# Kernel tuning notes

Hardware: AMD Instinct MI355X
Metric: run time of the kernel (lower is better)

Reference implementation:

```python
import math
import jax, jax.numpy as jnp
import numpy as np

N_NODES = 50000
N_EDGES = 800000
F_IN = 512
HID = 64
N_CLS = 64
NITER = 10


def setup_inputs() -> dict:
    key = jax.random.key(0)
    k = jax.random.split(key, 6)
    x = jax.random.normal(k[0], (N_NODES, F_IN), jnp.float32)
    edge_index = jax.random.randint(k[1], (2, N_EDGES), 0, N_NODES, jnp.int64)
    W1 = jax.random.normal(k[2], (F_IN, HID), jnp.float32) / np.sqrt(F_IN)
    b1 = jnp.zeros((HID,), jnp.float32)
    W2 = jax.random.normal(k[3], (HID, N_CLS), jnp.float32) / np.sqrt(HID)
    b2 = jnp.zeros((N_CLS,), jnp.float32)
    halt_w = jax.random.normal(k[4], (N_CLS,), jnp.float32) / np.sqrt(N_CLS)
    # reset_parameters: bias = log((1/(niter+1)) / (1 - 1/(niter+1)))
    b = math.log((1.0 / (NITER + 1)) / (1.0 - 1.0 / (NITER + 1)))
    halt_b = jnp.full((1,), b, jnp.float32)
    return {"x": x, "edge_index": edge_index, "W1": W1, "b1": b1,
            "W2": W2, "b2": b2, "halt_w": halt_w, "halt_b": halt_b}


def reference(x, edge_index, W1, b1, W2, b2, halt_w, halt_b):
    N = x.shape[0]
    # MLP (eval mode: dropout is identity)
    h = jnp.maximum(x @ W1 + b1, 0.0)
    local = h @ W2 + b2                      # [N, C] local predictions
    # GCN normalization with self-loops (eval: no edge dropout)
    loops = jnp.arange(N, dtype=edge_index.dtype)
    row = jnp.concatenate([edge_index[0], loops])
    col = jnp.concatenate([edge_index[1], loops])
    deg = jnp.zeros((N,), x.dtype).at[row].add(1.0)
    dis = jnp.where(deg > 0, jax.lax.rsqrt(jnp.maximum(deg, 1.0)), 0.0)
    norm = dis[row] * dis[col]               # [E+N]

    def step(carry, _):
        prop, steps, sum_h, cont, xacc = carry
        old = prop
        msg = norm[:, None] * prop[row]                       # gather + scale
        prop = jax.ops.segment_sum(msg, col, num_segments=N)  # scatter-add
        hh = jax.nn.sigmoid(prop @ halt_w + halt_b[0])        # [N]
        prob = (sum_h + hh < 0.99) & cont
        pf = prob.astype(x.dtype)
        steps = steps + pf
        sum_h = sum_h + pf * hh
        cond = prob & (steps < NITER)
        p = jnp.where(cond, sum_h, 1.0 - sum_h)
        xacc = xacc + (prop * p[:, None] + old * (1.0 - p)[:, None]) * cont.astype(x.dtype)[:, None]
        cont = cont & prob
        return (prop, steps, sum_h, cont, xacc), None

    init = (local, jnp.ones((N,), x.dtype), jnp.zeros((N,), x.dtype),
            jnp.ones((N,), bool), jnp.zeros_like(local))
    (prop, steps, sum_h, cont, xacc), _ = jax.lax.scan(step, init, None, length=NITER)
    out = xacc / steps[:, None]
    return jax.nn.log_softmax(out, axis=1), steps, 1.0 - sum_h
```

## Files before the change

kernel.cpp:

```cpp
#include <hip/hip_runtime.h>
#include <hip/hip_bf16.h>

#define F_IN 512
#define NC 64
#define NITER 10

__global__ __launch_bounds__(256) void init_state_kernel(
    float* __restrict__ steps, float* __restrict__ sumh, int* __restrict__ cont,
    int* __restrict__ rowptr, int N, int E) {
  int i = blockIdx.x * blockDim.x + threadIdx.x;
  if (i < N) { steps[i] = 1.0f; sumh[i] = 0.0f; cont[i] = 1; }
  if (i == 0) rowptr[N] = E;
}

__global__ __launch_bounds__(256) void mlp_kernel(
    const float* __restrict__ x, const float* __restrict__ W1,
    const float* __restrict__ b1, const float* __restrict__ W2,
    const float* __restrict__ b2, float* __restrict__ out, int N) {
  int r = blockIdx.x * blockDim.x + threadIdx.x;
  if (r >= N) return;
  const float* xr = x + (size_t)r * F_IN;
  float h[NC];
#pragma unroll
  for (int j = 0; j < NC; ++j) h[j] = b1[j];
  for (int k0 = 0; k0 < F_IN; k0 += 4) {
    float4 xv = *reinterpret_cast<const float4*>(xr + k0);
    float xs[4] = {xv.x, xv.y, xv.z, xv.w};
#pragma unroll
    for (int kk = 0; kk < 4; ++kk) {
      const float* w1row = W1 + (size_t)(k0 + kk) * NC;
      float xk = xs[kk];
#pragma unroll
      for (int j = 0; j < NC; ++j) h[j] = fmaf(xk, w1row[j], h[j]);
    }
  }
#pragma unroll
  for (int j = 0; j < NC; ++j) h[j] = fmaxf(h[j], 0.0f);
  float* orow = out + (size_t)r * NC;
#pragma unroll
  for (int jc = 0; jc < NC; jc += 16) {
    float o[16];
#pragma unroll
    for (int jj = 0; jj < 16; ++jj) o[jj] = b2[jc + jj];
    for (int m = 0; m < NC; ++m) {
      float hm = h[m];
      const float* w2row = W2 + (size_t)m * NC + jc;
#pragma unroll
      for (int jj = 0; jj < 16; ++jj) o[jj] = fmaf(hm, w2row[jj], o[jj]);
    }
#pragma unroll
    for (int jj = 0; jj < 16; ++jj) orow[jc + jj] = o[jj];
  }
}

__global__ __launch_bounds__(256) void hist_kernel(
    const int* __restrict__ ei, int* __restrict__ deg_i,
    int* __restrict__ indeg, int E) {
  int e = blockIdx.x * blockDim.x + threadIdx.x;
  if (e < E) {
    atomicAdd(&deg_i[ei[e]], 1);
    atomicAdd(&indeg[ei[E + e]], 1);
  }
}

__global__ __launch_bounds__(256) void dis_kernel(
    const int* __restrict__ deg_i, float* __restrict__ dis, int N) {
  int i = blockIdx.x * blockDim.x + threadIdx.x;
  if (i < N) dis[i] = 1.0f / sqrtf((float)(deg_i[i] + 1));
}

__global__ __launch_bounds__(256) void scan_sum_kernel(
    const int* __restrict__ indeg, int* __restrict__ bsum, int N) {
  __shared__ int sm[256];
  int tid = threadIdx.x;
  int i = blockIdx.x * 256 + tid;
  sm[tid] = (i < N) ? indeg[i] : 0;
  __syncthreads();
  for (int s = 128; s > 0; s >>= 1) {
    if (tid < s) sm[tid] += sm[tid + s];
    __syncthreads();
  }
  if (tid == 0) bsum[blockIdx.x] = sm[0];
}

__global__ __launch_bounds__(256) void scan_bsum_kernel(int* __restrict__ bsum, int nb) {
  __shared__ int sm[256];
  int tid = threadIdx.x;
  int v = (tid < nb) ? bsum[tid] : 0;
  sm[tid] = v;
  __syncthreads();
  for (int s = 1; s < 256; s <<= 1) {
    int t = (tid >= s) ? sm[tid - s] : 0;
    __syncthreads();
    sm[tid] += t;
    __syncthreads();
  }
  if (tid < nb) bsum[tid] = sm[tid] - v;
}

__global__ __launch_bounds__(256) void scan_final_kernel(
    const int* __restrict__ indeg, const int* __restrict__ bsum,
    int* __restrict__ rowptr, int N) {
  __shared__ int sm[256];
  int tid = threadIdx.x;
  int i = blockIdx.x * 256 + tid;
  int v = (i < N) ? indeg[i] : 0;
  sm[tid] = v;
  __syncthreads();
  for (int s = 1; s < 256; s <<= 1) {
    int t = (tid >= s) ? sm[tid - s] : 0;
    __syncthreads();
    sm[tid] += t;
    __syncthreads();
  }
  if (i < N) rowptr[i] = bsum[blockIdx.x] + sm[tid] - v;
}

__global__ __launch_bounds__(256) void scatter_kernel(
    const int* __restrict__ ei, const int* __restrict__ rowptr,
    int* __restrict__ cursor, const float* __restrict__ dis,
    int2* __restrict__ csr, int E) {
  int e = blockIdx.x * blockDim.x + threadIdx.x;
  if (e < E) {
    int s = ei[e];
    int c = ei[E + e];
    int pos = rowptr[c] + atomicAdd(&cursor[c], 1);
    csr[pos] = make_int2(s, __float_as_int(dis[s] * dis[c]));
  }
}

__global__ __launch_bounds__(256) void prop_step_kernel(
    const float* __restrict__ prop, float* __restrict__ prop_new,
    const int2* __restrict__ csr, const int* __restrict__ rowptr,
    const float* __restrict__ dis, const float* __restrict__ hw,
    const float* __restrict__ hb, float* __restrict__ steps,
    float* __restrict__ sumh, int* __restrict__ cont,
    float* __restrict__ xacc, int N) {
  int wid = (int)((blockIdx.x * blockDim.x + threadIdx.x) >> 6);
  if (wid >= N) return;
  int lane = threadIdx.x & 63;
  size_t rowoff = (size_t)wid * NC + lane;

  float oldv = prop[rowoff];
  float dc = dis[wid];
  int beg = __builtin_amdgcn_readfirstlane(rowptr[wid]);
  int end = __builtin_amdgcn_readfirstlane(rowptr[wid + 1]);

  float a0 = dc * dc * oldv, a1 = 0.f, a2 = 0.f, a3 = 0.f;
  int i = beg;
  for (; i + 4 <= end; i += 4) {
    int2 e0 = csr[i], e1 = csr[i + 1], e2 = csr[i + 2], e3 = csr[i + 3];
    a0 = fmaf(__int_as_float(e0.y), prop[(size_t)e0.x * NC + lane], a0);
    a1 = fmaf(__int_as_float(e1.y), prop[(size_t)e1.x * NC + lane], a1);
    a2 = fmaf(__int_as_float(e2.y), prop[(size_t)e2.x * NC + lane], a2);
    a3 = fmaf(__int_as_float(e3.y), prop[(size_t)e3.x * NC + lane], a3);
  }
  for (; i < end; ++i) {
    int2 e0 = csr[i];
    a0 = fmaf(__int_as_float(e0.y), prop[(size_t)e0.x * NC + lane], a0);
  }
  float acc = (a0 + a1) + (a2 + a3);
  prop_new[rowoff] = acc;

  float z = acc * hw[lane];
#pragma unroll
  for (int off = 32; off > 0; off >>= 1) z += __shfl_xor(z, off);
  z += hb[0];
  float hh = 1.0f / (1.0f + expf(-z));

  float st = steps[wid], sh = sumh[wid];
  int ct = cont[wid];
  bool prob = ((sh + hh) < 0.99f) && (ct != 0);
  float pf = prob ? 1.0f : 0.0f;
  st += pf;
  sh += pf * hh;
  bool cond = prob && (st < (float)NITER);
  float pp = cond ? sh : (1.0f - sh);
  float ctf = ct ? 1.0f : 0.0f;
  xacc[rowoff] += (acc * pp + oldv * (1.0f - pp)) * ctf;
  if (lane == 0) { steps[wid] = st; sumh[wid] = sh; cont[wid] = prob ? 1 : 0; }
}

__global__ __launch_bounds__(256) void final_kernel(
    const float* __restrict__ xacc, const float* __restrict__ steps,
    const float* __restrict__ sumh, float* __restrict__ out0,
    float* __restrict__ out1, float* __restrict__ out2, int N) {
  int wid = (int)((blockIdx.x * blockDim.x + threadIdx.x) >> 6);
  if (wid >= N) return;
  int lane = threadIdx.x & 63;
  float st = steps[wid];
  float v = xacc[(size_t)wid * NC + lane] / st;
  float m = v;
#pragma unroll
  for (int off = 32; off > 0; off >>= 1) m = fmaxf(m, __shfl_xor(m, off));
  float e = expf(v - m);
  float s = e;
#pragma unroll
  for (int off = 32; off > 0; off >>= 1) s += __shfl_xor(s, off);
  out0[(size_t)wid * NC + lane] = v - m - logf(s);
  if (lane == 0) { out1[wid] = st; out2[wid] = 1.0f - sumh[wid]; }
}

extern "C" void kernel_launch(void* const* d_in, const int* in_sizes, int n_in,
                              void* d_out, int out_size, void* d_ws, size_t ws_size,
                              hipStream_t stream) {
  const float* x      = (const float*)d_in[0];
  const int*   ei     = (const int*)d_in[1];
  const float* W1     = (const float*)d_in[2];
  const float* b1     = (const float*)d_in[3];
  const float* W2     = (const float*)d_in[4];
  const float* b2     = (const float*)d_in[5];
  const float* halt_w = (const float*)d_in[6];
  const float* halt_b = (const float*)d_in[7];

  const int N = in_sizes[0] / F_IN;
  const int E = in_sizes[1] / 2;

  char* p = (char*)d_ws;
  auto alloc = [&](size_t bytes) {
    void* r = (void*)p;
    p += (bytes + 255) & ~(size_t)255;
    return r;
  };
  float* propA  = (float*)alloc((size_t)N * NC * 4);
  float* propB  = (float*)alloc((size_t)N * NC * 4);
  float* xacc   = (float*)alloc((size_t)N * NC * 4);
  int2*  csr    = (int2*)alloc((size_t)E * 8);
  int*   rowptr = (int*)alloc((size_t)(N + 1) * 4);
  int*   deg_i  = (int*)alloc((size_t)N * 4);
  int*   indeg  = (int*)alloc((size_t)N * 4);
  int*   cursor = (int*)alloc((size_t)N * 4);
  float* dis    = (float*)alloc((size_t)N * 4);
  float* steps  = (float*)alloc((size_t)N * 4);
  float* sumh   = (float*)alloc((size_t)N * 4);
  int*   cont   = (int*)alloc((size_t)N * 4);
  int*   bsum   = (int*)alloc(1024);

  hipMemsetAsync(deg_i,  0, (size_t)N * 4, stream);
  hipMemsetAsync(indeg,  0, (size_t)N * 4, stream);
  hipMemsetAsync(cursor, 0, (size_t)N * 4, stream);
  hipMemsetAsync(xacc,   0, (size_t)N * NC * 4, stream);

  const int nbN = (N + 255) / 256;
  const int nbE = (E + 255) / 256;

  init_state_kernel<<<nbN, 256, 0, stream>>>(steps, sumh, cont, rowptr, N, E);
  mlp_kernel<<<nbN, 256, 0, stream>>>(x, W1, b1, W2, b2, propA, N);
  hist_kernel<<<nbE, 256, 0, stream>>>(ei, deg_i, indeg, E);
  dis_kernel<<<nbN, 256, 0, stream>>>(deg_i, dis, N);
  scan_sum_kernel<<<nbN, 256, 0, stream>>>(indeg, bsum, N);
  scan_bsum_kernel<<<1, 256, 0, stream>>>(bsum, nbN);
  scan_final_kernel<<<nbN, 256, 0, stream>>>(indeg, bsum, rowptr, N);
  scatter_kernel<<<nbE, 256, 0, stream>>>(ei, rowptr, cursor, dis, csr, E);

  float* out0 = (float*)d_out;
  float* out1 = out0 + (size_t)N * NC;
  float* out2 = out1 + N;

  const float* cur = propA;
  float* nxt = propB;
  const int nbW = (N + 3) / 4;
  for (int it = 0; it < NITER; ++it) {
    prop_step_kernel<<<nbW, 256, 0, stream>>>(cur, nxt, csr, rowptr, dis,
                                              halt_w, halt_b, steps, sumh,
                                              cont, xacc, N);
    const float* t = nxt; nxt = (float*)cur; cur = t;
  }
  final_kernel<<<nbW, 256, 0, stream>>>(xacc, steps, sumh, out0, out1, out2, N);
}
```

Measured before the change: 679.9 us.

## Rewrite MLP as shared-memory tiled GEMM with 8x4 register blocking

Replaces the one-row-per-thread MLP, which streamed a full x row per thread with poor coalescing and reloaded W1/W2 from global memory, with a block-tiled GEMM. Each block handles 128 rows: it stages transposed x tiles and W1 tiles in LDS, and each thread computes an 8x4 output tile. The hidden activations are then reused from LDS for the second layer. This raises coalescing and data reuse, at the cost of LDS use and extra barriers.

```diff
diff --git a/kernel.cpp b/kernel.cpp
--- a/kernel.cpp
+++ b/kernel.cpp
@@ -4,6 +4,9 @@
 #define F_IN 512
 #define NC 64
 #define NITER 10
+#define BM 128
+#define BK 64
+#define XS 132
 
 __global__ __launch_bounds__(256) void init_state_kernel(
     float* __restrict__ steps, float* __restrict__ sumh, int* __restrict__ cont,
@@ -17,39 +20,95 @@
     const float* __restrict__ x, const float* __restrict__ W1,
     const float* __restrict__ b1, const float* __restrict__ W2,
     const float* __restrict__ b2, float* __restrict__ out, int N) {
-  int r = blockIdx.x * blockDim.x + threadIdx.x;
-  if (r >= N) return;
-  const float* xr = x + (size_t)r * F_IN;
-  float h[NC];
-#pragma unroll
-  for (int j = 0; j < NC; ++j) h[j] = b1[j];
-  for (int k0 = 0; k0 < F_IN; k0 += 4) {
-    float4 xv = *reinterpret_cast<const float4*>(xr + k0);
-    float xs[4] = {xv.x, xv.y, xv.z, xv.w};
-#pragma unroll
-    for (int kk = 0; kk < 4; ++kk) {
-      const float* w1row = W1 + (size_t)(k0 + kk) * NC;
-      float xk = xs[kk];
-#pragma unroll
-      for (int j = 0; j < NC; ++j) h[j] = fmaf(xk, w1row[j], h[j]);
+  __shared__ float xT[BK * XS];
+  __shared__ float ws[BK * NC];
+  const int tid  = threadIdx.x;
+  const int brow = blockIdx.x * BM;
+  const int r0 = (tid >> 4) * 8;
+  const int c0 = (tid & 15) * 4;
+
+  float acc[8][4];
+#pragma unroll
+  for (int j = 0; j < 4; ++j) {
+    float bv = b1[c0 + j];
+#pragma unroll
+    for (int i = 0; i < 8; ++i) acc[i][j] = bv;
+  }
+
+  for (int kt = 0; kt < F_IN; kt += BK) {
+#pragma unroll
+    for (int q = 0; q < 8; ++q) {
+      int fidx = q * 256 + tid;
+      int row = fidx >> 4, kq = fidx & 15;
+      int gr = brow + row; if (gr >= N) gr = N - 1;
+      float4 v = *reinterpret_cast<const float4*>(&x[(size_t)gr * F_IN + kt + kq * 4]);
+      xT[(kq * 4 + 0) * XS + row] = v.x;
+      xT[(kq * 4 + 1) * XS + row] = v.y;
+      xT[(kq * 4 + 2) * XS + row] = v.z;
+      xT[(kq * 4 + 3) * XS + row] = v.w;
     }
-  }
-#pragma unroll
-  for (int j = 0; j < NC; ++j) h[j] = fmaxf(h[j], 0.0f);
-  float* orow = out + (size_t)r * NC;
-#pragma unroll
-  for (int jc = 0; jc < NC; jc += 16) {
-    float o[16];
-#pragma unroll
-    for (int jj = 0; jj < 16; ++jj) o[jj] = b2[jc + jj];
-    for (int m = 0; m < NC; ++m) {
-      float hm = h[m];
-      const float* w2row = W2 + (size_t)m * NC + jc;
-#pragma unroll
-      for (int jj = 0; jj < 16; ++jj) o[jj] = fmaf(hm, w2row[jj], o[jj]);
+#pragma unroll
+    for (int q = 0; q < 4; ++q) {
+      int fidx = q * 256 + tid;
+      int row = fidx >> 4, kq = fidx & 15;
+      *reinterpret_cast<float4*>(&ws[row * NC + kq * 4]) =
+          *reinterpret_cast<const float4*>(&W1[(size_t)(kt + row) * NC + kq * 4]);
     }
-#pragma unroll
-    for (int jj = 0; jj < 16; ++jj) orow[jc + jj] = o[jj];
+    __syncthreads();
+#pragma unroll 4
+    for (int k = 0; k < BK; ++k) {
+      float4 xa = *reinterpret_cast<const float4*>(&xT[k * XS + r0]);
+      float4 xb = *reinterpret_cast<const float4*>(&xT[k * XS + r0 + 4]);
+      float4 wv = *reinterpret_cast<const float4*>(&ws[k * NC + c0]);
+      float xr[8] = {xa.x, xa.y, xa.z, xa.w, xb.x, xb.y, xb.z, xb.w};
+      float wr[4] = {wv.x, wv.y, wv.z, wv.w};
+#pragma unroll
+      for (int i = 0; i < 8; ++i)
+#pragma unroll
+        for (int j = 0; j < 4; ++j) acc[i][j] = fmaf(xr[i], wr[j], acc[i][j]);
+    }
+    __syncthreads();
+  }
+
+#pragma unroll
+  for (int i = 0; i < 8; ++i)
+#pragma unroll
+    for (int j = 0; j < 4; ++j)
+      xT[(c0 + j) * XS + (r0 + i)] = fmaxf(acc[i][j], 0.0f);
+#pragma unroll
+  for (int q = 0; q < 4; ++q) {
+    int fidx = q * 256 + tid;
+    int row = fidx >> 4, kq = fidx & 15;
+    *reinterpret_cast<float4*>(&ws[row * NC + kq * 4]) =
+        *reinterpret_cast<const float4*>(&W2[(size_t)row * NC + kq * 4]);
+  }
+  float acc2[8][4];
+#pragma unroll
+  for (int j = 0; j < 4; ++j) {
+    float bv = b2[c0 + j];
+#pragma unroll
+    for (int i = 0; i < 8; ++i) acc2[i][j] = bv;
+  }
+  __syncthreads();
+#pragma unroll 4
+  for (int k = 0; k < NC; ++k) {
+    float4 xa = *reinterpret_cast<const float4*>(&xT[k * XS + r0]);
+    float4 xb = *reinterpret_cast<const float4*>(&xT[k * XS + r0 + 4]);
+    float4 wv = *reinterpret_cast<const float4*>(&ws[k * NC + c0]);
+    float xr[8] = {xa.x, xa.y, xa.z, xa.w, xb.x, xb.y, xb.z, xb.w};
+    float wr[4] = {wv.x, wv.y, wv.z, wv.w};
+#pragma unroll
+    for (int i = 0; i < 8; ++i)
+#pragma unroll
+      for (int j = 0; j < 4; ++j) acc2[i][j] = fmaf(xr[i], wr[j], acc2[i][j]);
+  }
+#pragma unroll
+  for (int i = 0; i < 8; ++i) {
+    int gr = brow + r0 + i;
+    if (gr < N) {
+      float4 o = make_float4(acc2[i][0], acc2[i][1], acc2[i][2], acc2[i][3]);
+      *reinterpret_cast<float4*>(&out[(size_t)gr * NC + c0]) = o;
+    }
   }
 }
 
@@ -243,9 +302,10 @@
 
   const int nbN = (N + 255) / 256;
   const int nbE = (E + 255) / 256;
+  const int nbM = (N + BM - 1) / BM;
 
   init_state_kernel<<<nbN, 256, 0, stream>>>(steps, sumh, cont, rowptr, N, E);
-  mlp_kernel<<<nbN, 256, 0, stream>>>(x, W1, b1, W2, b2, propA, N);
+  mlp_kernel<<<nbM, 256, 0, stream>>>(x, W1, b1, W2, b2, propA, N);
   hist_kernel<<<nbE, 256, 0, stream>>>(ei, deg_i, indeg, E);
   dis_kernel<<<nbN, 256, 0, stream>>>(deg_i, dis, N);
   scan_sum_kernel<<<nbN, 256, 0, stream>>>(indeg, bsum, N);
```

Result: faster. 588.1 us (-13.5%).
